# Optimization experiments

Hardware: AMD Instinct MI355X
Metric: run time of the kernel (lower is better)

Reference implementation:

```python
import jax, jax.numpy as jnp
import numpy as np

H = 16          # num_attention_heads
D = 1024        # hidden_size
HD = D // H     # attention_head_size = 64


def setup_inputs() -> dict:
    key = jax.random.key(0)
    ks = jax.random.split(key, 9)
    s = 1.0 / np.sqrt(D)
    return {
        "hidden_states": jax.random.normal(ks[0], (4, 1024, D), jnp.float32),
        "encoder_hidden_states": jax.random.normal(ks[1], (4, 1024, D), jnp.float32),
        "attention_mask": jnp.zeros((4, 1, 1, 2048), jnp.float32),
        "Wq": jax.random.normal(ks[2], (D, D), jnp.float32) * s,
        "bq": jnp.zeros((D,), jnp.float32),
        "Wk": jax.random.normal(ks[3], (D, D), jnp.float32) * s,
        "bk": jnp.zeros((D,), jnp.float32),
        "Wv": jax.random.normal(ks[4], (D, D), jnp.float32) * s,
        "bv": jnp.zeros((D,), jnp.float32),
    }


def _split_heads(x):
    # [B, S, D] -> [B, H, S, HD]
    B, S, _ = x.shape
    return x.reshape(B, S, H, HD).transpose(0, 2, 1, 3)


def reference(hidden_states, encoder_hidden_states, attention_mask, Wq, bq, Wk, bk, Wv, bv):
    # KV over concat(encoder, decoder); Q over decoder hidden states only.
    all_hidden = jnp.concatenate([encoder_hidden_states, hidden_states], axis=1)  # [B, Skv, D]
    q = _split_heads(hidden_states @ Wq + bq)        # [B, H, Sq, HD]
    k = _split_heads(all_hidden @ Wk + bk)           # [B, H, Skv, HD]
    v = _split_heads(all_hidden @ Wv + bv)           # [B, H, Skv, HD]

    scores = jnp.einsum("bhqd,bhkd->bhqk", q, k) / np.sqrt(HD).astype(np.float32)
    scores = scores + attention_mask                 # additive mask, broadcast
    probs = jax.nn.softmax(scores, axis=-1)          # dropout p=0 (eval)
    ctx = jnp.einsum("bhqk,bhkd->bhqd", probs, v)    # [B, H, Sq, HD]
    B, _, Sq, _ = ctx.shape
    return ctx.transpose(0, 2, 1, 3).reshape(B, Sq, D)
```

## Files before the change

### kernel.cpp

```cpp
#include <hip/hip_runtime.h>


typedef _Float16 f16;
typedef __attribute__((ext_vector_type(4))) _Float16 half4;
typedef __attribute__((ext_vector_type(8))) _Float16 half8;
typedef __attribute__((ext_vector_type(4))) float floatx4;
typedef __attribute__((ext_vector_type(16))) float floatx16;
typedef __attribute__((ext_vector_type(4))) unsigned int uint4v;

#define GLOAD16(gp, lp)                                                        \
    __builtin_amdgcn_global_load_lds(                                          \
        (const __attribute__((address_space(1))) void*)(gp),                   \
        (__attribute__((address_space(3))) void*)(lp), 16, 0, 0)

__global__ void prep_kernel(const float* __restrict__ hid, const float* __restrict__ enc,
                            const float* __restrict__ Wq, const float* __restrict__ Wk,
                            const float* __restrict__ Wv, f16* __restrict__ Wtq,
                            f16* __restrict__ Wtk, f16* __restrict__ Wtv,
                            f16* __restrict__ Aall) {
    int bid = blockIdx.x, tid = threadIdx.x;
    if (bid < 3072) {
        __shared__ float tile[32][33];
        int z = bid >> 10, xy = bid & 1023;
        const float* W = (z == 0) ? Wq : (z == 1) ? Wk : Wv;
        f16* Wt = (z == 0) ? Wtq : (z == 1) ? Wtk : Wtv;
        int n0 = (xy & 31) * 32, k0 = (xy >> 5) * 32;
        int tx = tid & 31, ty = tid >> 5;
        #pragma unroll
        for (int i = 0; i < 32; i += 8)
            tile[ty + i][tx] = W[(k0 + ty + i) * 1024 + n0 + tx];
        __syncthreads();
        #pragma unroll
        for (int i = 0; i < 32; i += 8)
            Wt[(n0 + ty + i) * 1024 + k0 + tx] = (f16)tile[tx][ty + i];
    } else {
        int t = (bid - 3072) * 256 + tid;
        int rowg = t >> 7, col = (t & 127) * 8;
        int b = rowg >> 11, r = rowg & 2047;
        const float* src = (r < 1024 ? enc + ((size_t)b * 1024 + r) * 1024
                                     : hid + ((size_t)b * 1024 + (r - 1024)) * 1024) + col;
        float4 v0 = *(const float4*)src, v1 = *(const float4*)(src + 4);
        half8 o;
        o[0] = (f16)v0.x; o[1] = (f16)v0.y; o[2] = (f16)v0.z; o[3] = (f16)v0.w;
        o[4] = (f16)v1.x; o[5] = (f16)v1.y; o[6] = (f16)v1.z; o[7] = (f16)v1.w;
        *(half8*)(Aall + (size_t)rowg * 1024 + col) = o;
    }
}

__launch_bounds__(256)
__global__ void qkv_gemm(const f16* __restrict__ Aall,
                         const f16* __restrict__ Wtq, const f16* __restrict__ Wtk,
                         const f16* __restrict__ Wtv,
                         const float* __restrict__ bq, const float* __restrict__ bk,
                         const float* __restrict__ bv,
                         f16* __restrict__ Qw, f16* __restrict__ Kw, f16* __restrict__ Vtw) {
    int mode = blockIdx.z;
    if (mode == 0 && blockIdx.x >= 32) return;
    __shared__ f16 As0[128 * 32];
    __shared__ f16 Bs0[128 * 32];
    __shared__ f16 As1[128 * 32];
    __shared__ f16 Bs1[128 * 32];
    __shared__ f16 As2[128 * 32];
    __shared__ f16 Bs2[128 * 32];

    const f16* Wt = (mode == 0) ? Wtq : (mode == 1) ? Wtk : Wtv;
    const float* bias = (mode == 0) ? bq : (mode == 1) ? bk : bv;
    f16* out = (mode == 0) ? Qw : (mode == 1) ? Kw : Vtw;

    int tid = threadIdx.x;
    int m0 = blockIdx.x * 128, n0 = blockIdx.y * 128;
    int wid = tid >> 6, lane = tid & 63;
    int wm = (wid >> 1) * 64, wn = (wid & 1) * 64;
    int lr = lane & 15, lg = lane >> 4;

    floatx4 acc[4][4];
    #pragma unroll
    for (int i = 0; i < 4; i++)
        #pragma unroll
        for (int j = 0; j < 4; j++) acc[i][j] = (floatx4)(0.f);

    int trow = tid >> 2;
    int tcol = (((tid & 3) ^ ((tid >> 3) & 3))) * 8;
    const f16 *a0g, *a1g;
    {
        int mA0 = m0 + trow, mA1 = mA0 + 64;
        if (mode == 0) {
            int b0 = mA0 >> 10, b1 = mA1 >> 10;
            a0g = Aall + ((size_t)(b0 * 2048 + 1024 + (mA0 & 1023))) * 1024 + tcol;
            a1g = Aall + ((size_t)(b1 * 2048 + 1024 + (mA1 & 1023))) * 1024 + tcol;
        } else {
            a0g = Aall + (size_t)mA0 * 1024 + tcol;
            a1g = Aall + (size_t)mA1 * 1024 + tcol;
        }
    }
    const f16* b0g = Wt + (size_t)(n0 + trow) * 1024 + tcol;
    const f16* b1g = Wt + (size_t)(n0 + trow + 64) * 1024 + tcol;

    int rcol = (lg ^ ((lr >> 1) & 3)) * 8;

    #define QKV_STAGE(off, Abuf, Bbuf)                    \
        GLOAD16(a0g + (off), &Abuf[tid * 8]);             \
        GLOAD16(a1g + (off), &Abuf[tid * 8 + 2048]);      \
        GLOAD16(b0g + (off), &Bbuf[tid * 8]);             \
        GLOAD16(b1g + (off), &Bbuf[tid * 8 + 2048]);

    #define QKV_COMPUTE(Abuf, Bbuf)                                                       \
        {                                                                                 \
            half8 a[4], bf[4];                                                            \
            _Pragma("unroll")                                                             \
            for (int i = 0; i < 4; i++)                                                   \
                a[i] = *(const half8*)&Abuf[(wm + i * 16 + lr) * 32 + rcol];              \
            _Pragma("unroll")                                                             \
            for (int j = 0; j < 4; j++)                                                   \
                bf[j] = *(const half8*)&Bbuf[(wn + j * 16 + lr) * 32 + rcol];             \
            __builtin_amdgcn_s_setprio(1);                                                \
            _Pragma("unroll")                                                             \
            for (int i = 0; i < 4; i++)                                                   \
                _Pragma("unroll")                                                         \
                for (int j = 0; j < 4; j++)                                               \
                    acc[i][j] = __builtin_amdgcn_mfma_f32_16x16x32_f16(a[i], bf[j],       \
                                                                      acc[i][j], 0, 0, 0);\
            __builtin_amdgcn_s_setprio(0);                                                \
        }

    QKV_STAGE(0,  As0, Bs0);
    QKV_STAGE(32, As1, Bs1);
    QKV_STAGE(64, As2, Bs2);
    asm volatile("s_waitcnt vmcnt(8)" ::: "memory");
    __builtin_amdgcn_s_barrier();

    for (int k0 = 0; k0 < 960; k0 += 96) {
        QKV_COMPUTE(As0, Bs0);
        asm volatile("s_waitcnt lgkmcnt(0)" ::: "memory");
        __builtin_amdgcn_s_barrier();
        QKV_STAGE(k0 + 96, As0, Bs0);
        asm volatile("s_waitcnt vmcnt(8)" ::: "memory");
        __builtin_amdgcn_s_barrier();

        QKV_COMPUTE(As1, Bs1);
        asm volatile("s_waitcnt lgkmcnt(0)" ::: "memory");
        __builtin_amdgcn_s_barrier();
        QKV_STAGE(k0 + 128, As1, Bs1);
        asm volatile("s_waitcnt vmcnt(8)" ::: "memory");
        __builtin_amdgcn_s_barrier();

        QKV_COMPUTE(As2, Bs2);
        asm volatile("s_waitcnt lgkmcnt(0)" ::: "memory");
        __builtin_amdgcn_s_barrier();
        if (k0 + 160 < 1024) {
            QKV_STAGE(k0 + 160, As2, Bs2);
            asm volatile("s_waitcnt vmcnt(8)" ::: "memory");
        } else {
            asm volatile("s_waitcnt vmcnt(4)" ::: "memory");
        }
        __builtin_amdgcn_s_barrier();
    }

    QKV_COMPUTE(As0, Bs0);
    asm volatile("s_waitcnt vmcnt(0)" ::: "memory");
    __builtin_amdgcn_s_barrier();
    QKV_COMPUTE(As1, Bs1);

    #undef QKV_STAGE
    #undef QKV_COMPUTE

    if (mode == 2) {
        #pragma unroll
        for (int i = 0; i < 4; i++) {
            int mbase = m0 + wm + i * 16 + lg * 4;
            int b = mbase >> 11, s = mbase & 2047;
            #pragma unroll
            for (int j = 0; j < 4; j++) {
                int n = n0 + wn + j * 16 + lr;
                int h = n >> 6, d = n & 63;
                float bv = bias[n];
                half4 w;
                #pragma unroll
                for (int r = 0; r < 4; r++) w[r] = (f16)(acc[i][j][r] + bv);
                *(half4*)(out + ((size_t)((b * 16 + h) * 64 + d)) * 2048 + s) = w;
            }
        }
    } else {
        int Sout = (mode == 0) ? 1024 : 2048;
        #pragma unroll
        for (int i = 0; i < 4; i++) {
            int mbase = m0 + wm + i * 16 + lg * 4;
            #pragma unroll
            for (int j = 0; j < 4; j++) {
                int n = n0 + wn + j * 16 + lr;
                int h = n >> 6, d = n & 63;
                float bv = bias[n];
                #pragma unroll
                for (int r = 0; r < 4; r++) {
                    int m = mbase + r;
                    int b = (mode == 0) ? (m >> 10) : (m >> 11);
                    int s = (mode == 0) ? (m & 1023) : (m & 2047);
                    out[((size_t)(b * 16 + h) * Sout + s) * 64 + d] = (f16)(acc[i][j][r] + bv);
                }
            }
        }
    }
}

__device__ inline half8 pack_swap(float s0, float s1, float s2, float s3,
                                  float s4, float s5, float s6, float s7) {
    unsigned a0 = __builtin_bit_cast(unsigned, __builtin_amdgcn_cvt_pkrtz(s0, s1));
    unsigned b0 = __builtin_bit_cast(unsigned, __builtin_amdgcn_cvt_pkrtz(s4, s5));
    unsigned a1 = __builtin_bit_cast(unsigned, __builtin_amdgcn_cvt_pkrtz(s2, s3));
    unsigned b1 = __builtin_bit_cast(unsigned, __builtin_amdgcn_cvt_pkrtz(s6, s7));
    asm("v_permlane32_swap_b32 %0, %1" : "+v"(a0), "+v"(b0));
    asm("v_permlane32_swap_b32 %0, %1" : "+v"(a1), "+v"(b1));
    uint4v w = {a0, a1, b0, b1};
    return __builtin_bit_cast(half8, w);
}

__device__ inline half8 pack_noswap(float s0, float s1, float s2, float s3,
                                    float s4, float s5, float s6, float s7) {
    unsigned w0 = __builtin_bit_cast(unsigned, __builtin_amdgcn_cvt_pkrtz(s0, s1));
    unsigned w1 = __builtin_bit_cast(unsigned, __builtin_amdgcn_cvt_pkrtz(s2, s3));
    unsigned w2 = __builtin_bit_cast(unsigned, __builtin_amdgcn_cvt_pkrtz(s4, s5));
    unsigned w3 = __builtin_bit_cast(unsigned, __builtin_amdgcn_cvt_pkrtz(s6, s7));
    uint4v w = {w0, w1, w2, w3};
    return __builtin_bit_cast(half8, w);
}

__launch_bounds__(256)
__global__ void attn_kernel(const f16* __restrict__ Q, const f16* __restrict__ K,
                            const f16* __restrict__ Vt, const float* __restrict__ mask,
                            float* __restrict__ out) {
    __shared__ f16 Kt[2][64 * 72];
    __shared__ f16 Vtt[2][64 * 72];
    __shared__ float maskLds[2048];

    const float LOG2E = 1.4426950408889634f;
    int tid = threadIdx.x;
    int wid = tid >> 6, lane = tid & 63;
    int l31 = lane & 31, l5 = lane >> 5;

    int bid = blockIdx.x + 8 * blockIdx.y;
    int xcd = bid & 7, w = bid >> 3;
    int bh = xcd * 8 + (w >> 3);
    int xblk = w & 7;
    int b = bh >> 4;
    int q = xblk * 128 + wid * 32 + l31;

    half8 pa, pcode;
    #pragma unroll
    for (int j = 0; j < 8; j++) { pa[j] = (f16)0; pcode[j] = (f16)(8 * l5 + j); }
    if (l31 < 16 && (l31 >> 3) == l5) pa[l31 & 7] = (f16)1;
    floatx16 pd = __builtin_amdgcn_mfma_f32_32x32x16_f16(pa, pcode, (floatx16)0.f, 0, 0, 0);
    float r4 = __shfl(pd[0], 32);
    bool twoblk = (r4 > 6.0f);

    const float* maskp = mask + b * 2048;
    for (int i = tid; i < 512; i += 256) {
        float4 mv = ((const float4*)maskp)[i];
        mv.x = mv.x * LOG2E - 8.0f; mv.y = mv.y * LOG2E - 8.0f;
        mv.z = mv.z * LOG2E - 8.0f; mv.w = mv.w * LOG2E - 8.0f;
        ((float4*)maskLds)[i] = mv;
    }

    const f16* qrow = Q + ((size_t)bh * 1024 + q) * 64;
    half8 qf[4];
    if (!twoblk) {
        #pragma unroll
        for (int ks = 0; ks < 4; ks++)
            qf[ks] = *(const half8*)(qrow + ks * 16 + l5 * 8);
    } else {
        #pragma unroll
        for (int ks = 0; ks < 4; ks++) {
            half4 lo = *(const half4*)(qrow + ks * 16 + 4 * l5);
            half4 hi = *(const half4*)(qrow + ks * 16 + 8 + 4 * l5);
            qf[ks][0] = lo[0]; qf[ks][1] = lo[1]; qf[ks][2] = lo[2]; qf[ks][3] = lo[3];
            qf[ks][4] = hi[0]; qf[ks][5] = hi[1]; qf[ks][6] = hi[2]; qf[ks][7] = hi[3];
        }
    }
    const f16 qs = (f16)(0.125f * 1.4426950408889634f);
    #pragma unroll
    for (int ks = 0; ks < 4; ks++)
        #pragma unroll
        for (int x = 0; x < 8; x++) qf[ks][x] *= qs;

    half8 aones;
    #pragma unroll
    for (int j = 0; j < 8; j++) aones[j] = (l31 == 0) ? (f16)1 : (f16)0;

    floatx16 o0 = (floatx16)0.f, o1 = (floatx16)0.f, o2 = (floatx16)0.f;

    int sr = tid >> 2, sc = (tid & 3) * 16;
    const f16* Ksrc = K + ((size_t)bh * 2048 + sr) * 64 + sc;
    const f16* Vsrc = Vt + ((size_t)(bh * 64 + sr)) * 2048 + sc;

    half8 rk0 = *(const half8*)(Ksrc);
    half8 rk1 = *(const half8*)(Ksrc + 8);
    half8 rv0 = *(const half8*)(Vsrc);
    half8 rv1 = *(const half8*)(Vsrc + 8);
    *(half8*)&Kt[0][sr * 72 + sc]      = rk0;
    *(half8*)&Kt[0][sr * 72 + sc + 8]  = rk1;
    *(half8*)&Vtt[0][sr * 72 + sc]     = rv0;
    *(half8*)&Vtt[0][sr * 72 + sc + 8] = rv1;
    rk0 = *(const half8*)(Ksrc + (size_t)64 * 64);
    rk1 = *(const half8*)(Ksrc + (size_t)64 * 64 + 8);
    rv0 = *(const half8*)(Vsrc + 64);
    rv1 = *(const half8*)(Vsrc + 64 + 8);
    __syncthreads();

    int cur = 0;
    for (int kv0 = 0; kv0 < 2048; kv0 += 64) {
        if (kv0 < 2048 - 64) {
            int nx = cur ^ 1;
            *(half8*)&Kt[nx][sr * 72 + sc]      = rk0;
            *(half8*)&Kt[nx][sr * 72 + sc + 8]  = rk1;
            *(half8*)&Vtt[nx][sr * 72 + sc]     = rv0;
            *(half8*)&Vtt[nx][sr * 72 + sc + 8] = rv1;
            if (kv0 < 2048 - 128) {
                rk0 = *(const half8*)(Ksrc + (size_t)(kv0 + 128) * 64);
                rk1 = *(const half8*)(Ksrc + (size_t)(kv0 + 128) * 64 + 8);
                rv0 = *(const half8*)(Vsrc + kv0 + 128);
                rv1 = *(const half8*)(Vsrc + kv0 + 128 + 8);
            }
        }

        floatx16 sf0, sf1;
        #pragma unroll
        for (int g = 0; g < 4; g++) {
            float4 mk0 = *(const float4*)&maskLds[kv0 + 8 * g + 4 * l5];
            float4 mk1 = *(const float4*)&maskLds[kv0 + 32 + 8 * g + 4 * l5];
            #pragma unroll
            for (int i = 0; i < 4; i++) {
                sf0[4 * g + i] = ((const float*)&mk0)[i];
                sf1[4 * g + i] = ((const float*)&mk1)[i];
            }
        }

        __builtin_amdgcn_s_setprio(1);
        #pragma unroll
        for (int ks = 0; ks < 4; ks++) {
            half8 k0 = *(const half8*)&Kt[cur][l31 * 72 + ks * 16 + l5 * 8];
            half8 k1 = *(const half8*)&Kt[cur][(32 + l31) * 72 + ks * 16 + l5 * 8];
            sf0 = __builtin_amdgcn_mfma_f32_32x32x16_f16(k0, qf[ks], sf0, 0, 0, 0);
            sf1 = __builtin_amdgcn_mfma_f32_32x32x16_f16(k1, qf[ks], sf1, 0, 0, 0);
        }
        __builtin_amdgcn_s_setprio(0);

        #pragma unroll
        for (int r = 0; r < 16; r++) {
            sf0[r] = exp2f(sf0[r]);
            sf1[r] = exp2f(sf1[r]);
        }

        half8 pb[4];
        if (!twoblk) {
            pb[0] = pack_swap(sf0[0], sf0[1], sf0[2], sf0[3], sf0[4], sf0[5], sf0[6], sf0[7]);
            pb[1] = pack_swap(sf0[8], sf0[9], sf0[10], sf0[11], sf0[12], sf0[13], sf0[14], sf0[15]);
            pb[2] = pack_swap(sf1[0], sf1[1], sf1[2], sf1[3], sf1[4], sf1[5], sf1[6], sf1[7]);
            pb[3] = pack_swap(sf1[8], sf1[9], sf1[10], sf1[11], sf1[12], sf1[13], sf1[14], sf1[15]);
        } else {
            pb[0] = pack_noswap(sf0[0], sf0[1], sf0[2], sf0[3], sf0[4], sf0[5], sf0[6], sf0[7]);
            pb[1] = pack_noswap(sf0[8], sf0[9], sf0[10], sf0[11], sf0[12], sf0[13], sf0[14], sf0[15]);
            pb[2] = pack_noswap(sf1[0], sf1[1], sf1[2], sf1[3], sf1[4], sf1[5], sf1[6], sf1[7]);
            pb[3] = pack_noswap(sf1[8], sf1[9], sf1[10], sf1[11], sf1[12], sf1[13], sf1[14], sf1[15]);
        }

        __builtin_amdgcn_s_setprio(1);
        #pragma unroll
        for (int kb = 0; kb < 4; kb++) {
            half8 v0 = *(const half8*)&Vtt[cur][l31 * 72 + kb * 16 + l5 * 8];
            half8 v1 = *(const half8*)&Vtt[cur][(32 + l31) * 72 + kb * 16 + l5 * 8];
            o0 = __builtin_amdgcn_mfma_f32_32x32x16_f16(v0, pb[kb], o0, 0, 0, 0);
            o1 = __builtin_amdgcn_mfma_f32_32x32x16_f16(v1, pb[kb], o1, 0, 0, 0);
            o2 = __builtin_amdgcn_mfma_f32_32x32x16_f16(aones, pb[kb], o2, 0, 0, 0);
        }
        __builtin_amdgcn_s_setprio(0);

        asm volatile("s_waitcnt lgkmcnt(0)" ::: "memory");
        __builtin_amdgcn_sched_barrier(0);
        __builtin_amdgcn_s_barrier();
        cur ^= 1;
    }

    float l_all = __shfl(o2[0], l31);
    int h = bh & 15;
    float inv = 1.f / l_all;
    float* orow = out + ((size_t)(b * 1024 + q)) * 1024 + h * 64;
    #pragma unroll
    for (int g = 0; g < 4; g++) {
        float4 r0 = {o0[4 * g] * inv, o0[4 * g + 1] * inv, o0[4 * g + 2] * inv, o0[4 * g + 3] * inv};
        float4 r1 = {o1[4 * g] * inv, o1[4 * g + 1] * inv, o1[4 * g + 2] * inv, o1[4 * g + 3] * inv};
        *(float4*)&orow[8 * g + 4 * l5]      = r0;
        *(float4*)&orow[32 + 8 * g + 4 * l5] = r1;
    }
}

extern "C" void kernel_launch(void* const* d_in, const int* in_sizes, int n_in,
                              void* d_out, int out_size, void* d_ws, size_t ws_size,
                              hipStream_t stream) {
    const float* hid  = (const float*)d_in[0];
    const float* enc  = (const float*)d_in[1];
    const float* mask = (const float*)d_in[2];
    const float* Wq   = (const float*)d_in[3];
    const float* bq   = (const float*)d_in[4];
    const float* Wk   = (const float*)d_in[5];
    const float* bk   = (const float*)d_in[6];
    const float* Wv   = (const float*)d_in[7];
    const float* bv   = (const float*)d_in[8];
    float* out = (float*)d_out;

    char* ws = (char*)d_ws;
    f16* Wtq  = (f16*)(ws + ((size_t)0 << 20));
    f16* Wtk  = (f16*)(ws + ((size_t)2 << 20));
    f16* Wtv  = (f16*)(ws + ((size_t)4 << 20));
    f16* Aall = (f16*)(ws + ((size_t)6 << 20));
    f16* Qw   = (f16*)(ws + ((size_t)22 << 20));
    f16* Kw   = (f16*)(ws + ((size_t)30 << 20));
    f16* Vtw  = (f16*)(ws + ((size_t)46 << 20));

    prep_kernel<<<7168, 256, 0, stream>>>(hid, enc, Wq, Wk, Wv, Wtq, Wtk, Wtv, Aall);

    qkv_gemm<<<dim3(64, 8, 3), 256, 0, stream>>>(Aall, Wtq, Wtk, Wtv, bq, bk, bv, Qw, Kw, Vtw);

    attn_kernel<<<dim3(8, 64), 256, 0, stream>>>(Qw, Kw, Vtw, mask, out);
}
```

Measured before the change: 142.9 us.

## Split attention KV range in two and merge partial outputs in a new kernel

Splits the 2048-long KV loop across two blocks per (batch, head, q-tile), so the grid doubles from 512 to 1024 blocks and fills more of the GPU's compute units. Each half writes unnormalised fp16 partial outputs plus its row-sum to workspace, and a new merge kernel adds the two halves, divides by the combined sum and writes fp32 output. The merge is valid without rescaling because the softmax uses a fixed offset of -8 in place of a running max. In exchange it adds a kernel launch, extra global traffic for the partial buffers, and fp16 rounding of the unnormalised partial accumulators.

```diff
diff --git a/kernel.cpp b/kernel.cpp
--- a/kernel.cpp
+++ b/kernel.cpp
@@ -7,6 +7,8 @@
 typedef __attribute__((ext_vector_type(4))) float floatx4;
 typedef __attribute__((ext_vector_type(16))) float floatx16;
 typedef __attribute__((ext_vector_type(4))) unsigned int uint4v;
+
+#define OPSTRIDE ((size_t)4194304)
 
 #define GLOAD16(gp, lp)                                                        \
     __builtin_amdgcn_global_load_lds(                                          \
@@ -227,19 +229,20 @@
 __launch_bounds__(256)
 __global__ void attn_kernel(const f16* __restrict__ Q, const f16* __restrict__ K,
                             const f16* __restrict__ Vt, const float* __restrict__ mask,
-                            float* __restrict__ out) {
+                            f16* __restrict__ Opart, float* __restrict__ lbuf) {
     __shared__ f16 Kt[2][64 * 72];
     __shared__ f16 Vtt[2][64 * 72];
-    __shared__ float maskLds[2048];
+    __shared__ float maskLds[1024];
 
     const float LOG2E = 1.4426950408889634f;
     int tid = threadIdx.x;
     int wid = tid >> 6, lane = tid & 63;
     int l31 = lane & 31, l5 = lane >> 5;
 
-    int bid = blockIdx.x + 8 * blockIdx.y;
+    int bid = blockIdx.x + 8 * blockIdx.y + 512 * blockIdx.z;
     int xcd = bid & 7, w = bid >> 3;
-    int bh = xcd * 8 + (w >> 3);
+    int unit = xcd * 16 + (w >> 3);
+    int bh = unit >> 1, sp = unit & 1;
     int xblk = w & 7;
     int b = bh >> 4;
     int q = xblk * 128 + wid * 32 + l31;
@@ -252,12 +255,11 @@
     float r4 = __shfl(pd[0], 32);
     bool twoblk = (r4 > 6.0f);
 
-    const float* maskp = mask + b * 2048;
-    for (int i = tid; i < 512; i += 256) {
-        float4 mv = ((const float4*)maskp)[i];
+    {
+        float4 mv = ((const float4*)(mask + b * 2048 + sp * 1024))[tid];
         mv.x = mv.x * LOG2E - 8.0f; mv.y = mv.y * LOG2E - 8.0f;
         mv.z = mv.z * LOG2E - 8.0f; mv.w = mv.w * LOG2E - 8.0f;
-        ((float4*)maskLds)[i] = mv;
+        ((float4*)maskLds)[tid] = mv;
     }
 
     const f16* qrow = Q + ((size_t)bh * 1024 + q) * 64;
@@ -288,8 +290,8 @@
     floatx16 o0 = (floatx16)0.f, o1 = (floatx16)0.f, o2 = (floatx16)0.f;
 
     int sr = tid >> 2, sc = (tid & 3) * 16;
-    const f16* Ksrc = K + ((size_t)bh * 2048 + sr) * 64 + sc;
-    const f16* Vsrc = Vt + ((size_t)(bh * 64 + sr)) * 2048 + sc;
+    const f16* Ksrc = K + ((size_t)(bh * 2048 + sp * 1024 + sr)) * 64 + sc;
+    const f16* Vsrc = Vt + ((size_t)(bh * 64 + sr)) * 2048 + sp * 1024 + sc;
 
     half8 rk0 = *(const half8*)(Ksrc);
     half8 rk1 = *(const half8*)(Ksrc + 8);
@@ -306,14 +308,14 @@
     __syncthreads();
 
     int cur = 0;
-    for (int kv0 = 0; kv0 < 2048; kv0 += 64) {
-        if (kv0 < 2048 - 64) {
+    for (int kv0 = 0; kv0 < 1024; kv0 += 64) {
+        if (kv0 < 1024 - 64) {
             int nx = cur ^ 1;
             *(half8*)&Kt[nx][sr * 72 + sc]      = rk0;
             *(half8*)&Kt[nx][sr * 72 + sc + 8]  = rk1;
             *(half8*)&Vtt[nx][sr * 72 + sc]     = rv0;
             *(half8*)&Vtt[nx][sr * 72 + sc + 8] = rv1;
-            if (kv0 < 2048 - 128) {
+            if (kv0 < 1024 - 128) {
                 rk0 = *(const half8*)(Ksrc + (size_t)(kv0 + 128) * 64);
                 rk1 = *(const half8*)(Ksrc + (size_t)(kv0 + 128) * 64 + 8);
                 rv0 = *(const half8*)(Vsrc + kv0 + 128);
@@ -379,17 +381,37 @@
         cur ^= 1;
     }
 
-    float l_all = __shfl(o2[0], l31);
-    int h = bh & 15;
-    float inv = 1.f / l_all;
-    float* orow = out + ((size_t)(b * 1024 + q)) * 1024 + h * 64;
+    size_t row = (size_t)bh * 1024 + q;
+    size_t obase = (size_t)sp * OPSTRIDE + row * 64;
     #pragma unroll
     for (int g = 0; g < 4; g++) {
-        float4 r0 = {o0[4 * g] * inv, o0[4 * g + 1] * inv, o0[4 * g + 2] * inv, o0[4 * g + 3] * inv};
-        float4 r1 = {o1[4 * g] * inv, o1[4 * g + 1] * inv, o1[4 * g + 2] * inv, o1[4 * g + 3] * inv};
-        *(float4*)&orow[8 * g + 4 * l5]      = r0;
-        *(float4*)&orow[32 + 8 * g + 4 * l5] = r1;
-    }
+        half4 w0, w1;
+        #pragma unroll
+        for (int r = 0; r < 4; r++) {
+            w0[r] = (f16)o0[4 * g + r];
+            w1[r] = (f16)o1[4 * g + r];
+        }
+        *(half4*)(Opart + obase + 8 * g + 4 * l5)      = w0;
+        *(half4*)(Opart + obase + 32 + 8 * g + 4 * l5) = w1;
+    }
+    if (l5 == 0) lbuf[(size_t)sp * 65536 + row] = o2[0];
+}
+
+__global__ void merge_kernel(const f16* __restrict__ Op, const float* __restrict__ lbuf,
+                             float* __restrict__ out) {
+    int t = blockIdx.x * 256 + threadIdx.x;
+    int row = t >> 3, dc = (t & 7) * 8;
+    int bh = row >> 10, q = row & 1023, b = bh >> 4, h = bh & 15;
+    float inv = 1.f / (lbuf[row] + lbuf[65536 + row]);
+    half8 a = *(const half8*)(Op + (size_t)row * 64 + dc);
+    half8 c = *(const half8*)(Op + OPSTRIDE + (size_t)row * 64 + dc);
+    float* orow = out + ((size_t)(b * 1024 + q)) * 1024 + h * 64 + dc;
+    float4 lo = {((float)a[0] + (float)c[0]) * inv, ((float)a[1] + (float)c[1]) * inv,
+                 ((float)a[2] + (float)c[2]) * inv, ((float)a[3] + (float)c[3]) * inv};
+    float4 hi = {((float)a[4] + (float)c[4]) * inv, ((float)a[5] + (float)c[5]) * inv,
+                 ((float)a[6] + (float)c[6]) * inv, ((float)a[7] + (float)c[7]) * inv};
+    *(float4*)orow = lo;
+    *(float4*)(orow + 4) = hi;
 }
 
 extern "C" void kernel_launch(void* const* d_in, const int* in_sizes, int n_in,
@@ -414,10 +436,13 @@
     f16* Qw   = (f16*)(ws + ((size_t)22 << 20));
     f16* Kw   = (f16*)(ws + ((size_t)30 << 20));
     f16* Vtw  = (f16*)(ws + ((size_t)46 << 20));
+    f16*   Opart = (f16*)(ws + ((size_t)0 << 20));
+    float* lbuf  = (float*)(ws + ((size_t)17 << 20));
 
     prep_kernel<<<7168, 256, 0, stream>>>(hid, enc, Wq, Wk, Wv, Wtq, Wtk, Wtv, Aall);
 
     qkv_gemm<<<dim3(64, 8, 3), 256, 0, stream>>>(Aall, Wtq, Wtk, Wtv, bq, bk, bv, Qw, Kw, Vtw);
 
-    attn_kernel<<<dim3(8, 64), 256, 0, stream>>>(Qw, Kw, Vtw, mask, out);
-}
+    attn_kernel<<<dim3(8, 64, 2), 256, 0, stream>>>(Qw, Kw, Vtw, mask, Opart, lbuf);
+    merge_kernel<<<2048, 256, 0, stream>>>(Opart, lbuf, out);
+}
```

After: 150.9 us. +5.6%, slower.

## Software-pipeline attention loop with 4-stage LDS ring and QK/PV overlap

Applied to the files above, without the earlier changes.

Replaces the double-buffered K/V LDS tiles with a four-buffer ring and restructures the KV loop so each tile's QK^T MFMA runs while the previous tile's exp/pack and PV MFMA run. Two score register sets alternate across the unrolled stages. The goal is to hide exp2 and LDS latency behind matrix work and keep global loads further ahead. In exchange it doubles K/V LDS use and raises register pressure, which may lower occupancy.

```diff
diff --git a/kernel.cpp b/kernel.cpp
--- a/kernel.cpp
+++ b/kernel.cpp
@@ -228,8 +228,8 @@
 __global__ void attn_kernel(const f16* __restrict__ Q, const f16* __restrict__ K,
                             const f16* __restrict__ Vt, const float* __restrict__ mask,
                             float* __restrict__ out) {
-    __shared__ f16 Kt[2][64 * 72];
-    __shared__ f16 Vtt[2][64 * 72];
+    __shared__ f16 Kt0[64 * 72], Kt1[64 * 72], Kt2[64 * 72], Kt3[64 * 72];
+    __shared__ f16 Vt0[64 * 72], Vt1[64 * 72], Vt2[64 * 72], Vt3[64 * 72];
     __shared__ float maskLds[2048];
 
     const float LOG2E = 1.4426950408889634f;
@@ -286,98 +286,130 @@
     for (int j = 0; j < 8; j++) aones[j] = (l31 == 0) ? (f16)1 : (f16)0;
 
     floatx16 o0 = (floatx16)0.f, o1 = (floatx16)0.f, o2 = (floatx16)0.f;
+    floatx16 sfA0, sfA1, sfB0, sfB1;
 
     int sr = tid >> 2, sc = (tid & 3) * 16;
     const f16* Ksrc = K + ((size_t)bh * 2048 + sr) * 64 + sc;
     const f16* Vsrc = Vt + ((size_t)(bh * 64 + sr)) * 2048 + sc;
 
-    half8 rk0 = *(const half8*)(Ksrc);
-    half8 rk1 = *(const half8*)(Ksrc + 8);
-    half8 rv0 = *(const half8*)(Vsrc);
-    half8 rv1 = *(const half8*)(Vsrc + 8);
-    *(half8*)&Kt[0][sr * 72 + sc]      = rk0;
-    *(half8*)&Kt[0][sr * 72 + sc + 8]  = rk1;
-    *(half8*)&Vtt[0][sr * 72 + sc]     = rv0;
-    *(half8*)&Vtt[0][sr * 72 + sc + 8] = rv1;
-    rk0 = *(const half8*)(Ksrc + (size_t)64 * 64);
-    rk1 = *(const half8*)(Ksrc + (size_t)64 * 64 + 8);
-    rv0 = *(const half8*)(Vsrc + 64);
-    rv1 = *(const half8*)(Vsrc + 64 + 8);
+    half8 rk0, rk1, rv0, rv1;
+
+    #define ATT_LOAD(kv)                                                        \
+        rk0 = *(const half8*)(Ksrc + (size_t)(kv) * 64);                        \
+        rk1 = *(const half8*)(Ksrc + (size_t)(kv) * 64 + 8);                    \
+        rv0 = *(const half8*)(Vsrc + (kv));                                     \
+        rv1 = *(const half8*)(Vsrc + (kv) + 8);
+
+    #define ATT_WRITE(KB, VB)                                                   \
+        *(half8*)&KB[sr * 72 + sc]     = rk0;                                   \
+        *(half8*)&KB[sr * 72 + sc + 8] = rk1;                                   \
+        *(half8*)&VB[sr * 72 + sc]     = rv0;                                   \
+        *(half8*)&VB[sr * 72 + sc + 8] = rv1;
+
+    #define ATT_F(KB, S0, S1, kv0)                                              \
+        {                                                                       \
+            _Pragma("unroll")                                                   \
+            for (int g = 0; g < 4; g++) {                                       \
+                float4 mk0 = *(const float4*)&maskLds[(kv0) + 8 * g + 4 * l5];  \
+                float4 mk1 = *(const float4*)&maskLds[(kv0) + 32 + 8 * g + 4 * l5]; \
+                _Pragma("unroll")                                               \
+                for (int i = 0; i < 4; i++) {                                   \
+                    S0[4 * g + i] = ((const float*)&mk0)[i];                    \
+                    S1[4 * g + i] = ((const float*)&mk1)[i];                    \
+                }                                                               \
+            }                                                                   \
+            __builtin_amdgcn_s_setprio(1);                                      \
+            _Pragma("unroll")                                                   \
+            for (int ks = 0; ks < 4; ks++) {                                    \
+                half8 k0 = *(const half8*)&KB[l31 * 72 + ks * 16 + l5 * 8];     \
+                half8 k1 = *(const half8*)&KB[(32 + l31) * 72 + ks * 16 + l5 * 8]; \
+                S0 = __builtin_amdgcn_mfma_f32_32x32x16_f16(k0, qf[ks], S0, 0, 0, 0); \
+                S1 = __builtin_amdgcn_mfma_f32_32x32x16_f16(k1, qf[ks], S1, 0, 0, 0); \
+            }                                                                   \
+            __builtin_amdgcn_s_setprio(0);                                      \
+        }
+
+    #define ATT_E(S0, S1, PB)                                                   \
+        {                                                                       \
+            _Pragma("unroll")                                                   \
+            for (int r = 0; r < 16; r++) {                                      \
+                S0[r] = exp2f(S0[r]);                                           \
+                S1[r] = exp2f(S1[r]);                                           \
+            }                                                                   \
+            if (!twoblk) {                                                      \
+                PB[0] = pack_swap(S0[0], S0[1], S0[2], S0[3], S0[4], S0[5], S0[6], S0[7]); \
+                PB[1] = pack_swap(S0[8], S0[9], S0[10], S0[11], S0[12], S0[13], S0[14], S0[15]); \
+                PB[2] = pack_swap(S1[0], S1[1], S1[2], S1[3], S1[4], S1[5], S1[6], S1[7]); \
+                PB[3] = pack_swap(S1[8], S1[9], S1[10], S1[11], S1[12], S1[13], S1[14], S1[15]); \
+            } else {                                                            \
+                PB[0] = pack_noswap(S0[0], S0[1], S0[2], S0[3], S0[4], S0[5], S0[6], S0[7]); \
+                PB[1] = pack_noswap(S0[8], S0[9], S0[10], S0[11], S0[12], S0[13], S0[14], S0[15]); \
+                PB[2] = pack_noswap(S1[0], S1[1], S1[2], S1[3], S1[4], S1[5], S1[6], S1[7]); \
+                PB[3] = pack_noswap(S1[8], S1[9], S1[10], S1[11], S1[12], S1[13], S1[14], S1[15]); \
+            }                                                                   \
+        }
+
+    #define ATT_P(VB, PB)                                                       \
+        {                                                                       \
+            __builtin_amdgcn_s_setprio(1);                                      \
+            _Pragma("unroll")                                                   \
+            for (int kb = 0; kb < 4; kb++) {                                    \
+                half8 v0 = *(const half8*)&VB[l31 * 72 + kb * 16 + l5 * 8];     \
+                half8 v1 = *(const half8*)&VB[(32 + l31) * 72 + kb * 16 + l5 * 8]; \
+                o0 = __builtin_amdgcn_mfma_f32_32x32x16_f16(v0, PB[kb], o0, 0, 0, 0); \
+                o1 = __builtin_amdgcn_mfma_f32_32x32x16_f16(v1, PB[kb], o1, 0, 0, 0); \
+                o2 = __builtin_amdgcn_mfma_f32_32x32x16_f16(aones, PB[kb], o2, 0, 0, 0); \
+            }                                                                   \
+            __builtin_amdgcn_s_setprio(0);                                      \
+        }
+
+    #define ATT_BARRIER()                                                       \
+        asm volatile("s_waitcnt lgkmcnt(0)" ::: "memory");                      \
+        __builtin_amdgcn_sched_barrier(0);                                      \
+        __builtin_amdgcn_s_barrier();
+
+    ATT_LOAD(0);   ATT_WRITE(Kt0, Vt0);
+    ATT_LOAD(64);  ATT_WRITE(Kt1, Vt1);
+    ATT_LOAD(128); ATT_WRITE(Kt2, Vt2);
+    ATT_LOAD(192);
     __syncthreads();
-
-    int cur = 0;
-    for (int kv0 = 0; kv0 < 2048; kv0 += 64) {
-        if (kv0 < 2048 - 64) {
-            int nx = cur ^ 1;
-            *(half8*)&Kt[nx][sr * 72 + sc]      = rk0;
-            *(half8*)&Kt[nx][sr * 72 + sc + 8]  = rk1;
-            *(half8*)&Vtt[nx][sr * 72 + sc]     = rv0;
-            *(half8*)&Vtt[nx][sr * 72 + sc + 8] = rv1;
-            if (kv0 < 2048 - 128) {
-                rk0 = *(const half8*)(Ksrc + (size_t)(kv0 + 128) * 64);
-                rk1 = *(const half8*)(Ksrc + (size_t)(kv0 + 128) * 64 + 8);
-                rv0 = *(const half8*)(Vsrc + kv0 + 128);
-                rv1 = *(const half8*)(Vsrc + kv0 + 128 + 8);
-            }
-        }
-
-        floatx16 sf0, sf1;
-        #pragma unroll
-        for (int g = 0; g < 4; g++) {
-            float4 mk0 = *(const float4*)&maskLds[kv0 + 8 * g + 4 * l5];
-            float4 mk1 = *(const float4*)&maskLds[kv0 + 32 + 8 * g + 4 * l5];
-            #pragma unroll
-            for (int i = 0; i < 4; i++) {
-                sf0[4 * g + i] = ((const float*)&mk0)[i];
-                sf1[4 * g + i] = ((const float*)&mk1)[i];
-            }
-        }
-
-        __builtin_amdgcn_s_setprio(1);
-        #pragma unroll
-        for (int ks = 0; ks < 4; ks++) {
-            half8 k0 = *(const half8*)&Kt[cur][l31 * 72 + ks * 16 + l5 * 8];
-            half8 k1 = *(const half8*)&Kt[cur][(32 + l31) * 72 + ks * 16 + l5 * 8];
-            sf0 = __builtin_amdgcn_mfma_f32_32x32x16_f16(k0, qf[ks], sf0, 0, 0, 0);
-            sf1 = __builtin_amdgcn_mfma_f32_32x32x16_f16(k1, qf[ks], sf1, 0, 0, 0);
-        }
-        __builtin_amdgcn_s_setprio(0);
-
-        #pragma unroll
-        for (int r = 0; r < 16; r++) {
-            sf0[r] = exp2f(sf0[r]);
-            sf1[r] = exp2f(sf1[r]);
-        }
-
-        half8 pb[4];
-        if (!twoblk) {
-            pb[0] = pack_swap(sf0[0], sf0[1], sf0[2], sf0[3], sf0[4], sf0[5], sf0[6], sf0[7]);
-            pb[1] = pack_swap(sf0[8], sf0[9], sf0[10], sf0[11], sf0[12], sf0[13], sf0[14], sf0[15]);
-            pb[2] = pack_swap(sf1[0], sf1[1], sf1[2], sf1[3], sf1[4], sf1[5], sf1[6], sf1[7]);
-            pb[3] = pack_swap(sf1[8], sf1[9], sf1[10], sf1[11], sf1[12], sf1[13], sf1[14], sf1[15]);
-        } else {
-            pb[0] = pack_noswap(sf0[0], sf0[1], sf0[2], sf0[3], sf0[4], sf0[5], sf0[6], sf0[7]);
-            pb[1] = pack_noswap(sf0[8], sf0[9], sf0[10], sf0[11], sf0[12], sf0[13], sf0[14], sf0[15]);
-            pb[2] = pack_noswap(sf1[0], sf1[1], sf1[2], sf1[3], sf1[4], sf1[5], sf1[6], sf1[7]);
-            pb[3] = pack_noswap(sf1[8], sf1[9], sf1[10], sf1[11], sf1[12], sf1[13], sf1[14], sf1[15]);
-        }
-
-        __builtin_amdgcn_s_setprio(1);
-        #pragma unroll
-        for (int kb = 0; kb < 4; kb++) {
-            half8 v0 = *(const half8*)&Vtt[cur][l31 * 72 + kb * 16 + l5 * 8];
-            half8 v1 = *(const half8*)&Vtt[cur][(32 + l31) * 72 + kb * 16 + l5 * 8];
-            o0 = __builtin_amdgcn_mfma_f32_32x32x16_f16(v0, pb[kb], o0, 0, 0, 0);
-            o1 = __builtin_amdgcn_mfma_f32_32x32x16_f16(v1, pb[kb], o1, 0, 0, 0);
-            o2 = __builtin_amdgcn_mfma_f32_32x32x16_f16(aones, pb[kb], o2, 0, 0, 0);
-        }
-        __builtin_amdgcn_s_setprio(0);
-
-        asm volatile("s_waitcnt lgkmcnt(0)" ::: "memory");
-        __builtin_amdgcn_sched_barrier(0);
-        __builtin_amdgcn_s_barrier();
-        cur ^= 1;
-    }
+    ATT_F(Kt0, sfA0, sfA1, 0);
+
+    half8 pb[4];
+    for (int g8 = 0; g8 < 8; g8++) {
+        int t4 = g8 * 4;
+        ATT_WRITE(Kt3, Vt3);
+        if (t4 + 4 < 32) { ATT_LOAD((t4 + 4) * 64); }
+        ATT_F(Kt1, sfB0, sfB1, (t4 + 1) * 64);
+        ATT_E(sfA0, sfA1, pb);
+        ATT_P(Vt0, pb);
+        ATT_BARRIER();
+        if (t4 + 4 < 32) { ATT_WRITE(Kt0, Vt0); }
+        if (t4 + 5 < 32) { ATT_LOAD((t4 + 5) * 64); }
+        ATT_F(Kt2, sfA0, sfA1, (t4 + 2) * 64);
+        ATT_E(sfB0, sfB1, pb);
+        ATT_P(Vt1, pb);
+        ATT_BARRIER();
+        if (t4 + 5 < 32) { ATT_WRITE(Kt1, Vt1); }
+        if (t4 + 6 < 32) { ATT_LOAD((t4 + 6) * 64); }
+        ATT_F(Kt3, sfB0, sfB1, (t4 + 3) * 64);
+        ATT_E(sfA0, sfA1, pb);
+        ATT_P(Vt2, pb);
+        ATT_BARRIER();
+        if (t4 + 6 < 32) { ATT_WRITE(Kt2, Vt2); }
+        if (t4 + 7 < 32) { ATT_LOAD((t4 + 7) * 64); }
+        if (t4 + 4 < 32) { ATT_F(Kt0, sfA0, sfA1, (t4 + 4) * 64); }
+        ATT_E(sfB0, sfB1, pb);
+        ATT_P(Vt3, pb);
+        ATT_BARRIER();
+    }
+
+    #undef ATT_LOAD
+    #undef ATT_WRITE
+    #undef ATT_F
+    #undef ATT_E
+    #undef ATT_P
+    #undef ATT_BARRIER
 
     float l_all = __shfl(o2[0], l31);
     int h = bh & 15;
```

After: 140.0 us, median of 2. 1.02x faster.
